# Kernel tuning notes

Measured on AMD Instinct MI355X. Metric: run time of the kernel, lower is better.

## Reference

```python
import jax, jax.numpy as jnp
import numpy as np

LAYER_NUM = 4
INPUT_DIM = 1024
BATCH = 16384


def setup_inputs() -> dict:
    key = jax.random.key(0)
    k1, k2, k3 = jax.random.split(key, 3)
    x = jax.random.normal(k1, (BATCH, INPUT_DIM), dtype=jnp.float32)
    cross_weights = jax.random.normal(k2, (LAYER_NUM, INPUT_DIM), dtype=jnp.float32)
    cross_bias = jax.random.normal(k3, (LAYER_NUM, INPUT_DIM), dtype=jnp.float32)
    return {"x": x, "cross_weights": cross_weights, "cross_bias": cross_bias}


def reference(x, cross_weights, cross_bias):
    # Faithful DCN cross network:
    #   x_{i+1} = x0 @ x_i^T @ w_i + b_i + x_i
    # The [B,d,d] outer product bmm collapses to a per-row scalar dot:
    #   x_{i+1} = x0 * (x_i . w_i) + b_i + x_i
    x0 = x
    xi = x
    for i in range(LAYER_NUM):
        s = xi @ cross_weights[i]            # [B]  (x_i^T w_i)
        xi = x0 * s[:, None] + cross_bias[i] + xi  # [B, d]
    return xi
```

## Files before the change

kernel.cpp:

```cpp
#include <hip/hip_runtime.h>


#define D 1024
#define LAYERS 4
#define CHUNKS 4

__global__ __launch_bounds__(256) void cross_network_kernel(
    const float* __restrict__ x,
    const float* __restrict__ w,
    const float* __restrict__ b,
    float* __restrict__ out,
    int batch)
{
    const int wave = (int)((blockIdx.x * blockDim.x + threadIdx.x) >> 6);
    const int lane = (int)(threadIdx.x & 63);
    if (wave >= batch) return;

    const float4* row = (const float4*)(x + (size_t)wave * D);

    float4 x0[CHUNKS], xi[CHUNKS];
#pragma unroll
    for (int c = 0; c < CHUNKS; ++c) {
        x0[c] = row[c * 64 + lane];
        xi[c] = x0[c];
    }

#pragma unroll
    for (int l = 0; l < LAYERS; ++l) {
        const float4* wl = (const float4*)(w + l * D);
        const float4* bl = (const float4*)(b + l * D);

        float s = 0.f;
#pragma unroll
        for (int c = 0; c < CHUNKS; ++c) {
            float4 wv = wl[c * 64 + lane];
            s = fmaf(xi[c].x, wv.x, s);
            s = fmaf(xi[c].y, wv.y, s);
            s = fmaf(xi[c].z, wv.z, s);
            s = fmaf(xi[c].w, wv.w, s);
        }
#pragma unroll
        for (int off = 32; off > 0; off >>= 1)
            s += __shfl_xor(s, off, 64);

#pragma unroll
        for (int c = 0; c < CHUNKS; ++c) {
            float4 bv = bl[c * 64 + lane];
            xi[c].x = fmaf(x0[c].x, s, bv.x + xi[c].x);
            xi[c].y = fmaf(x0[c].y, s, bv.y + xi[c].y);
            xi[c].z = fmaf(x0[c].z, s, bv.z + xi[c].z);
            xi[c].w = fmaf(x0[c].w, s, bv.w + xi[c].w);
        }
    }

    float4* orow = (float4*)(out + (size_t)wave * D);
#pragma unroll
    for (int c = 0; c < CHUNKS; ++c)
        orow[c * 64 + lane] = xi[c];
}

extern "C" void kernel_launch(void* const* d_in, const int* in_sizes, int n_in,
                              void* d_out, int out_size, void* d_ws, size_t ws_size,
                              hipStream_t stream) {
    const float* x = (const float*)d_in[0];
    const float* w = (const float*)d_in[1];
    const float* b = (const float*)d_in[2];
    float* out = (float*)d_out;

    const int batch = in_sizes[0] / D;
    const int waves_per_block = 256 / 64;
    const int grid = (batch + waves_per_block - 1) / waves_per_block;

    cross_network_kernel<<<grid, 256, 0, stream>>>(x, w, b, out, batch);
}
```

Measured before the change: 125.9 us.

## Collapse cross layers into one affine form with precomputed bias terms

Rewrites each layer output as a per-row scalar times x0 plus an accumulated bias vector. A small precompute kernel builds the bias prefix sum and the bias-weight dot products. The main kernel then computes all four x0·w dots in a single pass with one joint reduction. This removes the serial dependency between layers and the per-layer bias loads, at the cost of an extra kernel launch and some change in floating-point rounding order.

```diff
diff --git a/kernel.cpp b/kernel.cpp
--- a/kernel.cpp
+++ b/kernel.cpp
@@ -5,10 +5,58 @@
 #define LAYERS 4
 #define CHUNKS 4
 
-__global__ __launch_bounds__(256) void cross_network_kernel(
+__device__ inline float dot4(float4 a, float4 b) {
+    return fmaf(a.x, b.x, fmaf(a.y, b.y, fmaf(a.z, b.z, a.w * b.w)));
+}
+
+__global__ __launch_bounds__(256) void precompute_kernel(
+    const float* __restrict__ w,
+    const float* __restrict__ b,
+    float* __restrict__ ws)
+{
+    const int t = threadIdx.x;
+    const float4* b4 = (const float4*)b;
+    const float4* w4 = (const float4*)w;
+
+    float4 b0 = b4[t], b1 = b4[256 + t], b2 = b4[512 + t], b3 = b4[768 + t];
+    float4 w1 = w4[256 + t], w2 = w4[512 + t], w3 = w4[768 + t];
+
+    float4 s01, s012, bs;
+    s01.x = b0.x + b1.x;  s01.y = b0.y + b1.y;
+    s01.z = b0.z + b1.z;  s01.w = b0.w + b1.w;
+    s012.x = s01.x + b2.x; s012.y = s01.y + b2.y;
+    s012.z = s01.z + b2.z; s012.w = s01.w + b2.w;
+    bs.x = s012.x + b3.x; bs.y = s012.y + b3.y;
+    bs.z = s012.z + b3.z; bs.w = s012.w + b3.w;
+    ((float4*)ws)[t] = bs;
+
+    float g1 = dot4(b0, w1);
+    float g2 = dot4(s01, w2);
+    float g3 = dot4(s012, w3);
+
+#pragma unroll
+    for (int off = 32; off > 0; off >>= 1) {
+        g1 += __shfl_xor(g1, off, 64);
+        g2 += __shfl_xor(g2, off, 64);
+        g3 += __shfl_xor(g3, off, 64);
+    }
+
+    __shared__ float red[3][4];
+    const int wid = t >> 6, lane = t & 63;
+    if (lane == 0) { red[0][wid] = g1; red[1][wid] = g2; red[2][wid] = g3; }
+    __syncthreads();
+    if (t == 0) {
+        ws[D + 0] = 0.f;
+        ws[D + 1] = red[0][0] + red[0][1] + red[0][2] + red[0][3];
+        ws[D + 2] = red[1][0] + red[1][1] + red[1][2] + red[1][3];
+        ws[D + 3] = red[2][0] + red[2][1] + red[2][2] + red[2][3];
+    }
+}
+
+__global__ __launch_bounds__(256) void cross_main_kernel(
     const float* __restrict__ x,
     const float* __restrict__ w,
-    const float* __restrict__ b,
+    const float* __restrict__ ws,
     float* __restrict__ out,
     int batch)
 {
@@ -17,46 +65,58 @@
     if (wave >= batch) return;
 
     const float4* row = (const float4*)(x + (size_t)wave * D);
+    const float4* w4  = (const float4*)w;
+    const float4* bs4 = (const float4*)ws;
 
-    float4 x0[CHUNKS], xi[CHUNKS];
+    float4 x0[CHUNKS];
+#pragma unroll
+    for (int c = 0; c < CHUNKS; ++c) x0[c] = row[c * 64 + lane];
+
+    float d0 = 0.f, d1 = 0.f, d2 = 0.f, d3 = 0.f;
 #pragma unroll
     for (int c = 0; c < CHUNKS; ++c) {
-        x0[c] = row[c * 64 + lane];
-        xi[c] = x0[c];
+        const int idx = c * 64 + lane;
+        float4 wv0 = w4[idx];
+        float4 wv1 = w4[256 + idx];
+        float4 wv2 = w4[512 + idx];
+        float4 wv3 = w4[768 + idx];
+        d0 = fmaf(x0[c].x, wv0.x, d0); d1 = fmaf(x0[c].x, wv1.x, d1);
+        d2 = fmaf(x0[c].x, wv2.x, d2); d3 = fmaf(x0[c].x, wv3.x, d3);
+        d0 = fmaf(x0[c].y, wv0.y, d0); d1 = fmaf(x0[c].y, wv1.y, d1);
+        d2 = fmaf(x0[c].y, wv2.y, d2); d3 = fmaf(x0[c].y, wv3.y, d3);
+        d0 = fmaf(x0[c].z, wv0.z, d0); d1 = fmaf(x0[c].z, wv1.z, d1);
+        d2 = fmaf(x0[c].z, wv2.z, d2); d3 = fmaf(x0[c].z, wv3.z, d3);
+        d0 = fmaf(x0[c].w, wv0.w, d0); d1 = fmaf(x0[c].w, wv1.w, d1);
+        d2 = fmaf(x0[c].w, wv2.w, d2); d3 = fmaf(x0[c].w, wv3.w, d3);
     }
 
 #pragma unroll
-    for (int l = 0; l < LAYERS; ++l) {
-        const float4* wl = (const float4*)(w + l * D);
-        const float4* bl = (const float4*)(b + l * D);
+    for (int off = 32; off > 0; off >>= 1) {
+        d0 += __shfl_xor(d0, off, 64);
+        d1 += __shfl_xor(d1, off, 64);
+        d2 += __shfl_xor(d2, off, 64);
+        d3 += __shfl_xor(d3, off, 64);
+    }
 
-        float s = 0.f;
-#pragma unroll
-        for (int c = 0; c < CHUNKS; ++c) {
-            float4 wv = wl[c * 64 + lane];
-            s = fmaf(xi[c].x, wv.x, s);
-            s = fmaf(xi[c].y, wv.y, s);
-            s = fmaf(xi[c].z, wv.z, s);
-            s = fmaf(xi[c].w, wv.w, s);
-        }
-#pragma unroll
-        for (int off = 32; off > 0; off >>= 1)
-            s += __shfl_xor(s, off, 64);
+    const float g1 = ws[D + 1], g2 = ws[D + 2], g3 = ws[D + 3];
 
-#pragma unroll
-        for (int c = 0; c < CHUNKS; ++c) {
-            float4 bv = bl[c * 64 + lane];
-            xi[c].x = fmaf(x0[c].x, s, bv.x + xi[c].x);
-            xi[c].y = fmaf(x0[c].y, s, bv.y + xi[c].y);
-            xi[c].z = fmaf(x0[c].z, s, bv.z + xi[c].z);
-            xi[c].w = fmaf(x0[c].w, s, bv.w + xi[c].w);
-        }
-    }
+    float c1 = 1.f + d0;
+    float c2 = c1 + fmaf(c1, d1, g1);
+    float c3 = c2 + fmaf(c2, d2, g2);
+    float c4 = c3 + fmaf(c3, d3, g3);
 
     float4* orow = (float4*)(out + (size_t)wave * D);
 #pragma unroll
-    for (int c = 0; c < CHUNKS; ++c)
-        orow[c * 64 + lane] = xi[c];
+    for (int c = 0; c < CHUNKS; ++c) {
+        const int idx = c * 64 + lane;
+        float4 bs = bs4[idx];
+        float4 o;
+        o.x = fmaf(c4, x0[c].x, bs.x);
+        o.y = fmaf(c4, x0[c].y, bs.y);
+        o.z = fmaf(c4, x0[c].z, bs.z);
+        o.w = fmaf(c4, x0[c].w, bs.w);
+        orow[idx] = o;
+    }
 }
 
 extern "C" void kernel_launch(void* const* d_in, const int* in_sizes, int n_in,
@@ -66,10 +126,13 @@
     const float* w = (const float*)d_in[1];
     const float* b = (const float*)d_in[2];
     float* out = (float*)d_out;
+    float* ws  = (float*)d_ws;
 
     const int batch = in_sizes[0] / D;
+
+    precompute_kernel<<<1, 256, 0, stream>>>(w, b, ws);
+
     const int waves_per_block = 256 / 64;
     const int grid = (batch + waves_per_block - 1) / waves_per_block;
-
-    cross_network_kernel<<<grid, 256, 0, stream>>>(x, w, b, out, batch);
+    cross_main_kernel<<<grid, 256, 0, stream>>>(x, w, (const float*)ws, out, batch);
 }
```

Result: no change. 124.3 us (-1.3%).

## Collapse cross layers algebraically and pipeline multiple rows per wave

Applied to the files above, without the earlier changes.

Rewrites the four-layer recurrence so each output row is a scalar c4 times x0 plus a precomputed bias sum. The scalar comes from four independent dot products of x0 with the weights and three bias-weight constants computed once per wave. Each wave now handles four rows, prefetching the next row while computing the current one, and writes output with nontemporal stores. This removes the serial layer dependency and per-layer bias loads, but changes floating-point summation order and adds per-wave setup work.

```diff
diff --git a/kernel.cpp b/kernel.cpp
--- a/kernel.cpp
+++ b/kernel.cpp
@@ -2,61 +2,119 @@
 
 
 #define D 1024
-#define LAYERS 4
 #define CHUNKS 4
+#define ITER 4
 
-__global__ __launch_bounds__(256) void cross_network_kernel(
+typedef float nfloat4 __attribute__((ext_vector_type(4)));
+
+__global__ __launch_bounds__(256) void cross_pipe_kernel(
     const float* __restrict__ x,
     const float* __restrict__ w,
     const float* __restrict__ b,
     float* __restrict__ out,
     int batch)
 {
-    const int wave = (int)((blockIdx.x * blockDim.x + threadIdx.x) >> 6);
+    const int wid  = (int)((blockIdx.x * blockDim.x + threadIdx.x) >> 6);
     const int lane = (int)(threadIdx.x & 63);
-    if (wave >= batch) return;
+    const int row0 = wid * ITER;
+    if (row0 >= batch) return;
 
-    const float4* row = (const float4*)(x + (size_t)wave * D);
+    const float4* w4 = (const float4*)w;
+    const float4* b4 = (const float4*)b;
 
-    float4 x0[CHUNKS], xi[CHUNKS];
+    float g1 = 0.f, g2 = 0.f, g3 = 0.f;
+    float4 Bsum[CHUNKS];
 #pragma unroll
     for (int c = 0; c < CHUNKS; ++c) {
-        x0[c] = row[c * 64 + lane];
-        xi[c] = x0[c];
+        const int idx = c * 64 + lane;
+        float4 bb0 = b4[idx], bb1 = b4[256 + idx];
+        float4 bb2 = b4[512 + idx], bb3 = b4[768 + idx];
+        float4 wv1 = w4[256 + idx], wv2 = w4[512 + idx], wv3 = w4[768 + idx];
+
+        float4 B2, B3, Bs;
+        B2.x = bb0.x + bb1.x; B2.y = bb0.y + bb1.y;
+        B2.z = bb0.z + bb1.z; B2.w = bb0.w + bb1.w;
+        B3.x = B2.x + bb2.x;  B3.y = B2.y + bb2.y;
+        B3.z = B2.z + bb2.z;  B3.w = B2.w + bb2.w;
+        Bs.x = B3.x + bb3.x;  Bs.y = B3.y + bb3.y;
+        Bs.z = B3.z + bb3.z;  Bs.w = B3.w + bb3.w;
+        Bsum[c] = Bs;
+
+        g1 = fmaf(bb0.x, wv1.x, g1); g1 = fmaf(bb0.y, wv1.y, g1);
+        g1 = fmaf(bb0.z, wv1.z, g1); g1 = fmaf(bb0.w, wv1.w, g1);
+        g2 = fmaf(B2.x,  wv2.x, g2); g2 = fmaf(B2.y,  wv2.y, g2);
+        g2 = fmaf(B2.z,  wv2.z, g2); g2 = fmaf(B2.w,  wv2.w, g2);
+        g3 = fmaf(B3.x,  wv3.x, g3); g3 = fmaf(B3.y,  wv3.y, g3);
+        g3 = fmaf(B3.z,  wv3.z, g3); g3 = fmaf(B3.w,  wv3.w, g3);
+    }
+#pragma unroll
+    for (int off = 32; off > 0; off >>= 1) {
+        g1 += __shfl_xor(g1, off, 64);
+        g2 += __shfl_xor(g2, off, 64);
+        g3 += __shfl_xor(g3, off, 64);
     }
 
+    float4 xc[CHUNKS], xn[CHUNKS];
+    {
+        const float4* row = (const float4*)(x + (size_t)row0 * D);
 #pragma unroll
-    for (int l = 0; l < LAYERS; ++l) {
-        const float4* wl = (const float4*)(w + l * D);
-        const float4* bl = (const float4*)(b + l * D);
+        for (int c = 0; c < CHUNKS; ++c) xc[c] = row[c * 64 + lane];
+    }
 
-        float s = 0.f;
+#pragma unroll 1
+    for (int i = 0; i < ITER; ++i) {
+        const int rowi = row0 + i;
+        const int nrow = (rowi + 1 < batch) ? (rowi + 1) : rowi;
+        const float4* nrp = (const float4*)(x + (size_t)nrow * D);
+#pragma unroll
+        for (int c = 0; c < CHUNKS; ++c) xn[c] = nrp[c * 64 + lane];
+
+        float d0 = 0.f, d1 = 0.f, d2 = 0.f, d3 = 0.f;
 #pragma unroll
         for (int c = 0; c < CHUNKS; ++c) {
-            float4 wv = wl[c * 64 + lane];
-            s = fmaf(xi[c].x, wv.x, s);
-            s = fmaf(xi[c].y, wv.y, s);
-            s = fmaf(xi[c].z, wv.z, s);
-            s = fmaf(xi[c].w, wv.w, s);
+            const int idx = c * 64 + lane;
+            float4 wv0 = w4[idx];
+            float4 wv1 = w4[256 + idx];
+            float4 wv2 = w4[512 + idx];
+            float4 wv3 = w4[768 + idx];
+            d0 = fmaf(xc[c].x, wv0.x, d0); d1 = fmaf(xc[c].x, wv1.x, d1);
+            d2 = fmaf(xc[c].x, wv2.x, d2); d3 = fmaf(xc[c].x, wv3.x, d3);
+            d0 = fmaf(xc[c].y, wv0.y, d0); d1 = fmaf(xc[c].y, wv1.y, d1);
+            d2 = fmaf(xc[c].y, wv2.y, d2); d3 = fmaf(xc[c].y, wv3.y, d3);
+            d0 = fmaf(xc[c].z, wv0.z, d0); d1 = fmaf(xc[c].z, wv1.z, d1);
+            d2 = fmaf(xc[c].z, wv2.z, d2); d3 = fmaf(xc[c].z, wv3.z, d3);
+            d0 = fmaf(xc[c].w, wv0.w, d0); d1 = fmaf(xc[c].w, wv1.w, d1);
+            d2 = fmaf(xc[c].w, wv2.w, d2); d3 = fmaf(xc[c].w, wv3.w, d3);
         }
-#pragma unroll
-        for (int off = 32; off > 0; off >>= 1)
-            s += __shfl_xor(s, off, 64);
 
 #pragma unroll
+        for (int off = 32; off > 0; off >>= 1) {
+            d0 += __shfl_xor(d0, off, 64);
+            d1 += __shfl_xor(d1, off, 64);
+            d2 += __shfl_xor(d2, off, 64);
+            d3 += __shfl_xor(d3, off, 64);
+        }
+
+        float c1 = 1.f + d0;
+        float c2 = c1 + fmaf(c1, d1, g1);
+        float c3 = c2 + fmaf(c2, d2, g2);
+        float c4 = c3 + fmaf(c3, d3, g3);
+
+        nfloat4* orow = (nfloat4*)(out + (size_t)rowi * D);
+#pragma unroll
         for (int c = 0; c < CHUNKS; ++c) {
-            float4 bv = bl[c * 64 + lane];
-            xi[c].x = fmaf(x0[c].x, s, bv.x + xi[c].x);
-            xi[c].y = fmaf(x0[c].y, s, bv.y + xi[c].y);
-            xi[c].z = fmaf(x0[c].z, s, bv.z + xi[c].z);
-            xi[c].w = fmaf(x0[c].w, s, bv.w + xi[c].w);
+            const int idx = c * 64 + lane;
+            nfloat4 o;
+            o.x = fmaf(c4, xc[c].x, Bsum[c].x);
+            o.y = fmaf(c4, xc[c].y, Bsum[c].y);
+            o.z = fmaf(c4, xc[c].z, Bsum[c].z);
+            o.w = fmaf(c4, xc[c].w, Bsum[c].w);
+            __builtin_nontemporal_store(o, &orow[idx]);
         }
+
+#pragma unroll
+        for (int c = 0; c < CHUNKS; ++c) xc[c] = xn[c];
     }
-
-    float4* orow = (float4*)(out + (size_t)wave * D);
-#pragma unroll
-    for (int c = 0; c < CHUNKS; ++c)
-        orow[c * 64 + lane] = xi[c];
 }
 
 extern "C" void kernel_launch(void* const* d_in, const int* in_sizes, int n_in,
@@ -68,8 +126,7 @@
     float* out = (float*)d_out;
 
     const int batch = in_sizes[0] / D;
-    const int waves_per_block = 256 / 64;
-    const int grid = (batch + waves_per_block - 1) / waves_per_block;
-
-    cross_network_kernel<<<grid, 256, 0, stream>>>(x, w, b, out, batch);
+    const int rows_per_block = ITER * (256 / 64);
+    const int grid = (batch + rows_per_block - 1) / rows_per_block;
+    cross_pipe_kernel<<<grid, 256, 0, stream>>>(x, w, b, out, batch);
 }
```

New measurement: 119.4 us. 5.2% less time.
